# Performance work log

Measured on AMD Instinct MI355X. Metric: run time of the kernel, lower is better.

## Reference

```python
import jax, jax.numpy as jnp
import numpy as np
from jax import lax

N, T, E, A, D, S, O = 64, 2048, 512, 256, 512, 64, 80
R_ATT, R_FAC = 10, 2
H4 = 4 * D  # LSTM hidden size = 2048


def softsign(x):
    return x / (1.0 + jnp.abs(x))


def lstm_cell(x, h, c, Wih, Whh, bih, bhh):
    gates = x @ Wih.T + bih + h @ Whh.T + bhh
    i, f, g, o = jnp.split(gates, 4, axis=-1)  # torch gate order i,f,g,o
    c_new = jax.nn.sigmoid(f) * c + jax.nn.sigmoid(i) * jnp.tanh(g)
    h_new = jax.nn.sigmoid(o) * jnp.tanh(c_new)
    return h_new, c_new


def setup_inputs() -> dict:
    key = jax.random.key(0)
    ks = jax.random.split(key, 24)
    f = lambda k, shape, s=0.05: jax.random.normal(k, shape, dtype=jnp.float32) * s
    return {
        'input_enc': f(ks[0], (N, T, E), 1.0),
        'input_dec': f(ks[1], (N, O), 1.0),
        'spkr_vec': f(ks[2], (N, 1, S), 1.0),
        'speed': jax.random.uniform(ks[3], (N,), dtype=jnp.float32),
        'lengths_enc': jnp.full((N,), T, dtype=jnp.int32),
        'We': f(ks[4], (E, A)), 'be': jnp.zeros((A,), jnp.float32),
        'Ws': f(ks[5], (S, A)),
        'conv_w': f(ks[6], (A, 1, 31)),
        'w_proj': f(ks[7], (A,)), 'b_proj': jnp.zeros((), jnp.float32),
        'W_speed': f(ks[8], (A,)),
        'sp_W1': f(ks[9], (D,)), 'sp_b1': jnp.zeros((D,), jnp.float32),
        'sp_W2': f(ks[10], (D, E)), 'sp_b2': jnp.zeros((E,), jnp.float32),
        'pre_W1': f(ks[11], (O + S, 2 * D)), 'pre_b1': jnp.zeros((2 * D,), jnp.float32),
        'pre_W2': f(ks[12], (2 * D, D)), 'pre_b2': jnp.zeros((D,), jnp.float32),
        'Wih0': f(ks[13], (4 * H4, E + D + S)), 'Whh0': f(ks[14], (4 * H4, H4)),
        'bih0': jnp.zeros((4 * H4,), jnp.float32), 'bhh0': jnp.zeros((4 * H4,), jnp.float32),
        'Wih1': f(ks[15], (4 * H4, H4)), 'Whh1': f(ks[16], (4 * H4, H4)),
        'bih1': jnp.zeros((4 * H4,), jnp.float32), 'bhh1': jnp.zeros((4 * H4,), jnp.float32),
        'Wo': f(ks[17], (H4 + E, O * R_FAC)), 'bo': jnp.zeros((O * R_FAC,), jnp.float32),
    }


def _forward(input_enc, input_dec, spkr_vec, speed, lengths_enc,
             We, be, Ws, conv_w, w_proj, b_proj, W_speed,
             sp_W1, sp_b1, sp_W2, sp_b2,
             pre_W1, pre_b1, pre_W2, pre_b2,
             Wih0, Whh0, bih0, bhh0, Wih1, Whh1, bih1, bhh1, Wo, bo):
    n, t_enc, _ = input_enc.shape
    # first decoding step: previous attention = one-hot at t=0
    att0 = jnp.zeros((n, t_enc), jnp.float32).at[:, 0].set(1.0)
    bias_speed = (speed[:, None] * W_speed[None, :])[:, None, :]            # (N,1,A)
    bias_enc = softsign(jnp.einsum('nte,ea->nta', input_enc, We) + be)      # (N,T,A)
    bias_spkr = softsign(jnp.einsum('nse,ea->nsa', spkr_vec, Ws))           # (N,1,A)
    # prenet (dropout = identity at inference)
    x = jnp.concatenate([input_dec, spkr_vec[:, 0, :]], axis=-1)
    p = jax.nn.relu(jax.nn.relu(x @ pre_W1 + pre_b1) @ pre_W2 + pre_b2)     # (N,D)
    out_prenet = p[:, None, :]
    # location feature: conv1d(1->A, k=31, pad=15) over previous attention
    conv = lax.conv_general_dilated(att0[:, None, :], conv_w, (1,), [(15, 15)],
                                    dimension_numbers=('NCH', 'OIH', 'NCH'))
    conv = conv.transpose(0, 2, 1)                                          # (N,T,A)
    e = bias_enc + bias_spkr + conv + bias_speed                            # (N,T,A)
    # sliding-window mask around previous argmax, indices clamped to [0, len-1]
    m = jnp.argmax(att0, axis=1)                                            # (N,)
    L1 = (lengths_enc - 1).astype(m.dtype)
    i = jnp.arange(R_ATT)
    up = jnp.minimum(m[:, None] + i, L1[:, None])
    lo = jnp.minimum(jnp.maximum(m[:, None] - i, 0), L1[:, None])
    idx = jnp.concatenate([up, lo], axis=1)                                 # (N,2R)
    mask = jnp.zeros((n, t_enc), jnp.float32).at[jnp.arange(n)[:, None], idx].set(1.0)
    logit = jnp.einsum('nta,a->nt', jnp.tanh(e), w_proj) + b_proj           # (N,T)
    w = jnp.exp(logit - jnp.max(logit, axis=1, keepdims=True)) * mask
    att = w / jnp.maximum(jnp.sum(w, axis=1, keepdims=True), 1e-12)         # L1 normalize
    # speed-conditioned encoder shift
    sp = jnp.tanh(jax.nn.relu(speed[:, None] * sp_W1 + sp_b1) @ sp_W2 + sp_b2)  # (N,E)
    enc = input_enc + sp[:, None, :]
    context = jnp.einsum('nt,nte->ne', att, enc)[:, None, :]                # (N,1,E)
    in_lstm = jnp.concatenate([out_prenet, context, spkr_vec], axis=2)[:, 0, :]
    h0 = jnp.zeros((n, H4), jnp.float32)
    h1, _ = lstm_cell(in_lstm, h0, h0, Wih0, Whh0, bih0, bhh0)
    h2, _ = lstm_cell(h1, h0, h0, Wih1, Whh1, bih1, bhh1)
    dec_output = jnp.concatenate([h2[:, None, :], context], axis=2)         # (N,1,H4+E)
    output = (dec_output @ Wo + bo).reshape(n, R_FAC, -1)                   # (N,r,O)
    return output, context, dec_output


def reference(input_enc, input_dec, spkr_vec, speed, lengths_enc,
              We, be, Ws, conv_w, w_proj, b_proj, W_speed,
              sp_W1, sp_b1, sp_W2, sp_b2,
              pre_W1, pre_b1, pre_W2, pre_b2,
              Wih0, Whh0, bih0, bhh0, Wih1, Whh1, bih1, bhh1, Wo, bo):
    return _forward(input_enc, input_dec, spkr_vec, speed, lengths_enc,
                    We, be, Ws, conv_w, w_proj, b_proj, W_speed,
                    sp_W1, sp_b1, sp_W2, sp_b2,
                    pre_W1, pre_b1, pre_W2, pre_b2,
                    Wih0, Whh0, bih0, bhh0, Wih1, Whh1, bih1, bhh1, Wo, bo)
```

## Files before the change

kernel.cpp:

```cpp
#include <hip/hip_runtime.h>
#include <math.h>


__device__ __forceinline__ float sigmoidf_(float x){ return 1.0f/(1.0f+expf(-x)); }
__device__ __forceinline__ float softsignf_(float x){ return x/(1.0f+fabsf(x)); }

__device__ __forceinline__ void llds16(const float* g, float* l)
{
    __builtin_amdgcn_global_load_lds(
        (const __attribute__((address_space(1))) unsigned int*)g,
        (__attribute__((address_space(3))) unsigned int*)l, 16, 0, 0);
}


__global__ void hidden_kernel(const float* __restrict__ input_dec, const float* __restrict__ spkr,
                              const float* __restrict__ W, const float* __restrict__ b,
                              float* __restrict__ hid)
{
    const int n = blockIdx.x;
    const int j = blockIdx.y * 256 + threadIdx.x;
    float a0=0.f, a1=0.f, a2=0.f, a3=0.f;
    #pragma unroll 4
    for (int k = 0; k < 144; k += 4) {
        const float x0 = (k+0 < 80) ? input_dec[n*80 + k+0] : spkr[n*64 + (k+0-80)];
        const float x1 = (k+1 < 80) ? input_dec[n*80 + k+1] : spkr[n*64 + (k+1-80)];
        const float x2 = (k+2 < 80) ? input_dec[n*80 + k+2] : spkr[n*64 + (k+2-80)];
        const float x3 = (k+3 < 80) ? input_dec[n*80 + k+3] : spkr[n*64 + (k+3-80)];
        a0 = fmaf(x0, W[(k+0)*1024 + j], a0);
        a1 = fmaf(x1, W[(k+1)*1024 + j], a1);
        a2 = fmaf(x2, W[(k+2)*1024 + j], a2);
        a3 = fmaf(x3, W[(k+3)*1024 + j], a3);
    }
    hid[n*1024 + j] = fmaxf((a0+a1)+(a2+a3) + b[j], 0.f);
}

__global__ void sp_kernel(const float* __restrict__ speed, const float* __restrict__ sp_W1,
                          const float* __restrict__ sp_b1, const float* __restrict__ sp_W2,
                          const float* __restrict__ sp_b2, float* __restrict__ sp)
{
    const int n = blockIdx.x;
    const int j = blockIdx.y * 256 + threadIdx.x;
    const float s = speed[n];
    float a0=0.f, a1=0.f, a2=0.f, a3=0.f;
    #pragma unroll 4
    for (int d = 0; d < 512; d += 4) {
        const float r0 = fmaxf(fmaf(s, sp_W1[d+0], sp_b1[d+0]), 0.f);
        const float r1 = fmaxf(fmaf(s, sp_W1[d+1], sp_b1[d+1]), 0.f);
        const float r2 = fmaxf(fmaf(s, sp_W1[d+2], sp_b1[d+2]), 0.f);
        const float r3 = fmaxf(fmaf(s, sp_W1[d+3], sp_b1[d+3]), 0.f);
        a0 = fmaf(r0, sp_W2[(d+0)*512 + j], a0);
        a1 = fmaf(r1, sp_W2[(d+1)*512 + j], a1);
        a2 = fmaf(r2, sp_W2[(d+2)*512 + j], a2);
        a3 = fmaf(r3, sp_W2[(d+3)*512 + j], a3);
    }
    sp[n*512 + j] = tanhf((a0+a1)+(a2+a3) + sp_b2[j]);
}

__global__ void p_kernel(const float* __restrict__ hid, const float* __restrict__ W,
                         const float* __restrict__ b, float* __restrict__ xT0)
{
    const int n = blockIdx.x;
    const int j = blockIdx.y * 256 + threadIdx.x;
    const float* xr = hid + n*1024;
    float a0=0.f, a1=0.f, a2=0.f, a3=0.f;
    #pragma unroll 4
    for (int k = 0; k < 1024; k += 4) {
        a0 = fmaf(xr[k+0], W[(k+0)*512 + j], a0);
        a1 = fmaf(xr[k+1], W[(k+1)*512 + j], a1);
        a2 = fmaf(xr[k+2], W[(k+2)*512 + j], a2);
        a3 = fmaf(xr[k+3], W[(k+3)*512 + j], a3);
    }
    xT0[j*64 + n] = fmaxf((a0+a1)+(a2+a3) + b[j], 0.f);
}

__global__ void attn_kernel(const float* __restrict__ input_enc,
                            const float* __restrict__ spkr,
                            const float* __restrict__ speed,
                            const int*   __restrict__ lengths,
                            const float* __restrict__ We,
                            const float* __restrict__ be,
                            const float* __restrict__ Ws,
                            const float* __restrict__ conv_w,
                            const float* __restrict__ w_proj,
                            const float* __restrict__ b_proj,
                            const float* __restrict__ W_speed,
                            const float* __restrict__ sp,
                            float* __restrict__ xT0,
                            float* __restrict__ out_ctx,
                            float* __restrict__ out_dec)
{
    const int n = blockIdx.x;
    const int a = threadIdx.x;
    __shared__ float encs[10*512];
    __shared__ float part[4][10];
    __shared__ float logit_s[10];
    __shared__ float att_s[10];

    const int L1 = lengths[n] - 1;
    const int tc = (L1 + 1 < 10) ? (L1 + 1) : 10;
    const float sn = speed[n];
    const float* enc_n = input_enc + (size_t)n * (2048*512);

    for (int idx = a; idx < 10*512; idx += 256) encs[idx] = enc_n[idx];
    __syncthreads();

    float ds = 0.f;
    for (int s = 0; s < 64; ++s) ds = fmaf(spkr[n*64 + s], Ws[s*256 + a], ds);
    const float bspkr = softsignf_(ds);
    const float bspd  = sn * W_speed[a];
    const float bea   = be[a];
    const float wpa   = w_proj[a];

    float dt[10];
    #pragma unroll
    for (int t = 0; t < 10; ++t) dt[t] = 0.f;
    for (int k = 0; k < 512; ++k) {
        const float w = We[k*256 + a];
        #pragma unroll
        for (int t = 0; t < 10; ++t) dt[t] = fmaf(encs[t*512 + k], w, dt[t]);
    }

    for (int t = 0; t < 10; ++t) {
        float e = softsignf_(dt[t] + bea);
        e += bspkr + conv_w[a*31 + (15 - t)] + bspd;
        float v = tanhf(e) * wpa;
        #pragma unroll
        for (int off = 32; off > 0; off >>= 1) v += __shfl_down(v, off);
        if ((a & 63) == 0) part[a >> 6][t] = v;
    }
    __syncthreads();
    if (a < 10) logit_s[a] = part[0][a] + part[1][a] + part[2][a] + part[3][a] + b_proj[0];
    __syncthreads();
    if (a == 0) {
        float mx = -1e30f;
        for (int t = 0; t < tc; ++t) mx = fmaxf(mx, logit_s[t]);
        float ssum = 0.f;
        for (int t = 0; t < tc; ++t) { att_s[t] = expf(logit_s[t] - mx); ssum += att_s[t]; }
        const float inv = 1.f / fmaxf(ssum, 1e-12f);
        for (int t = 0; t < tc; ++t) att_s[t] *= inv;
        for (int t = tc; t < 10; ++t) att_s[t] = 0.f;
    }
    __syncthreads();

    for (int e0 = a; e0 < 512; e0 += 256) {
        const float spv = sp[n*512 + e0];
        float c = 0.f;
        for (int t = 0; t < tc; ++t) c = fmaf(att_s[t], encs[t*512 + e0] + spv, c);
        xT0[(512 + e0)*64 + n] = c;
        out_ctx[n*512 + e0]   = c;
        out_dec[n*2560 + 2048 + e0] = c;
    }
    if (a < 64) xT0[(1024 + a)*64 + n] = spkr[n*64 + a];
}

#define FMA_ROW(acc, wv) do { \
    acc.x = fmaf(wv.x, xk0.x, acc.x); acc.y = fmaf(wv.x, xk0.y, acc.y); \
    acc.z = fmaf(wv.x, xk0.z, acc.z); acc.w = fmaf(wv.x, xk0.w, acc.w); \
    acc.x = fmaf(wv.y, xk1.x, acc.x); acc.y = fmaf(wv.y, xk1.y, acc.y); \
    acc.z = fmaf(wv.y, xk1.z, acc.z); acc.w = fmaf(wv.y, xk1.w, acc.w); \
    acc.x = fmaf(wv.z, xk2.x, acc.x); acc.y = fmaf(wv.z, xk2.y, acc.y); \
    acc.z = fmaf(wv.z, xk2.z, acc.z); acc.w = fmaf(wv.z, xk2.w, acc.w); \
    acc.x = fmaf(wv.w, xk3.x, acc.x); acc.y = fmaf(wv.w, xk3.y, acc.y); \
    acc.z = fmaf(wv.w, xk3.z, acc.z); acc.w = fmaf(wv.w, xk3.w, acc.w); \
} while(0)

template<int K>
__global__ __launch_bounds__(256, 2)
void gemm_tile(const float* __restrict__ xT, const float* __restrict__ W,
               float* __restrict__ part)
{
    __shared__ __align__(16) float Wl[2][64*64];
    __shared__ __align__(16) float Xl[2][64*64];
    const int tid  = threadIdx.x;
    const int lane = tid & 63;
    const int w    = tid >> 6;
    const int tx   = tid & 15;
    const int ty   = tid >> 4;
    const int jjbase = blockIdx.x * 64;
    const int sy     = blockIdx.y;
    const int jg     = jjbase + ((jjbase >= 2048) ? 2048 : 0);

    constexpr int NT = K / 64;
    constexpr int NTQ = NT / 4, NTR = NT % 4;
    const int tn = NTQ + (sy < NTR ? 1 : 0);
    const int t0 = sy * NTQ + (sy < NTR ? sy : NTR);

    float4 a0 = {0,0,0,0}, a1 = {0,0,0,0}, a2 = {0,0,0,0}, a3 = {0,0,0,0};

    auto stage = [&](int t, int b) {
        const int k0 = t * 64;
        #pragma unroll
        for (int c = 0; c < 4; ++c) {
            const int u = w * 4 + c;
            llds16(xT + (size_t)k0 * 64 + u * 256 + lane * 4, &Xl[b][u * 256]);
            const int r0 = u * 4;
            llds16(W + (size_t)(jg + r0 + (lane >> 4)) * K + k0 + (lane & 15) * 4,
                   &Wl[b][r0 * 64]);
        }
    };

    stage(t0, 0);
    __syncthreads();

    for (int tt = 0; tt < tn; ++tt) {
        const int cur = tt & 1;
        if (tt + 1 < tn) stage(t0 + tt + 1, cur ^ 1);
        const float* Wc = Wl[cur];
        const float* Xc = Xl[cur];
        #pragma unroll
        for (int kk = 0; kk < 64; kk += 4) {
            const float4 xk0 = *(const float4*)(Xc + (kk+0)*64 + tx*4);
            const float4 xk1 = *(const float4*)(Xc + (kk+1)*64 + tx*4);
            const float4 xk2 = *(const float4*)(Xc + (kk+2)*64 + tx*4);
            const float4 xk3 = *(const float4*)(Xc + (kk+3)*64 + tx*4);
            const float4 w0 = *(const float4*)(Wc + (ty*4+0)*64 + kk);
            FMA_ROW(a0, w0);
            const float4 w1 = *(const float4*)(Wc + (ty*4+1)*64 + kk);
            FMA_ROW(a1, w1);
            const float4 w2 = *(const float4*)(Wc + (ty*4+2)*64 + kk);
            FMA_ROW(a2, w2);
            const float4 w3 = *(const float4*)(Wc + (ty*4+3)*64 + kk);
            FMA_ROW(a3, w3);
        }
        __syncthreads();
    }

    float* op = part + (size_t)(sy * 6144 + jjbase) * 64;
    *(float4*)(op + (ty*4+0)*64 + tx*4) = a0;
    *(float4*)(op + (ty*4+1)*64 + tx*4) = a1;
    *(float4*)(op + (ty*4+2)*64 + tx*4) = a2;
    *(float4*)(op + (ty*4+3)*64 + tx*4) = a3;
}

__global__ void lstm_act_kernel(const float* __restrict__ part,
                                const float* __restrict__ b1, const float* __restrict__ b2,
                                float* __restrict__ hT, float* __restrict__ dec_out)
{
    const int idx = blockIdx.x * 256 + threadIdx.x;
    const int n = idx & 63;
    const int m = idx >> 6;
    float gi = b1[m]        + b2[m];
    float gg = b1[4096 + m] + b2[4096 + m];
    float go = b1[6144 + m] + b2[6144 + m];
    #pragma unroll
    for (int s = 0; s < 4; ++s) {
        gi += part[(size_t)(s * 6144 +        m) * 64 + n];
        gg += part[(size_t)(s * 6144 + 2048 + m) * 64 + n];
        go += part[(size_t)(s * 6144 + 4096 + m) * 64 + n];
    }
    const float c = sigmoidf_(gi) * tanhf(gg);
    const float h = sigmoidf_(go) * tanhf(c);
    hT[idx] = h;
    if (dec_out) dec_out[n*2560 + m] = h;
}

__global__ void final_partial_kernel(const float* __restrict__ h2T, const float* __restrict__ ctx,
                                     const float* __restrict__ Wo, float* __restrict__ part)
{
    const int n  = blockIdx.x;
    const int kc = blockIdx.y;
    const int j  = threadIdx.x;
    if (j >= 160) return;
    const int k0 = kc * 128;
    float a0=0.f, a1=0.f, a2=0.f, a3=0.f;
    if (kc < 16) {
        #pragma unroll 4
        for (int k = k0; k < k0 + 128; k += 4) {
            a0 = fmaf(h2T[(k+0)*64 + n], Wo[(k+0)*160 + j], a0);
            a1 = fmaf(h2T[(k+1)*64 + n], Wo[(k+1)*160 + j], a1);
            a2 = fmaf(h2T[(k+2)*64 + n], Wo[(k+2)*160 + j], a2);
            a3 = fmaf(h2T[(k+3)*64 + n], Wo[(k+3)*160 + j], a3);
        }
    } else {
        const float* cr = ctx + n*512;
        #pragma unroll 4
        for (int k = k0; k < k0 + 128; k += 4) {
            a0 = fmaf(cr[k+0-2048], Wo[(k+0)*160 + j], a0);
            a1 = fmaf(cr[k+1-2048], Wo[(k+1)*160 + j], a1);
            a2 = fmaf(cr[k+2-2048], Wo[(k+2)*160 + j], a2);
            a3 = fmaf(cr[k+3-2048], Wo[(k+3)*160 + j], a3);
        }
    }
    part[(kc*64 + n)*160 + j] = (a0+a1)+(a2+a3);
}

__global__ void final_reduce_kernel(const float* __restrict__ part, const float* __restrict__ bo,
                                    float* __restrict__ out)
{
    const int idx = blockIdx.x * 256 + threadIdx.x;
    const int j = idx - (idx / 160) * 160;
    float s = bo[j];
    #pragma unroll
    for (int kc = 0; kc < 20; ++kc) s += part[kc*10240 + idx];
    out[idx] = s;
}

extern "C" void kernel_launch(void* const* d_in, const int* in_sizes, int n_in,
                              void* d_out, int out_size, void* d_ws, size_t ws_size,
                              hipStream_t stream)
{
    const float* input_enc = (const float*)d_in[0];
    const float* input_dec = (const float*)d_in[1];
    const float* spkr      = (const float*)d_in[2];
    const float* speed     = (const float*)d_in[3];
    const int*   lengths   = (const int*)  d_in[4];
    const float* We        = (const float*)d_in[5];
    const float* be        = (const float*)d_in[6];
    const float* Ws        = (const float*)d_in[7];
    const float* conv_w    = (const float*)d_in[8];
    const float* w_proj    = (const float*)d_in[9];
    const float* b_proj    = (const float*)d_in[10];
    const float* W_speed   = (const float*)d_in[11];
    const float* sp_W1     = (const float*)d_in[12];
    const float* sp_b1     = (const float*)d_in[13];
    const float* sp_W2     = (const float*)d_in[14];
    const float* sp_b2     = (const float*)d_in[15];
    const float* pre_W1    = (const float*)d_in[16];
    const float* pre_b1    = (const float*)d_in[17];
    const float* pre_W2    = (const float*)d_in[18];
    const float* pre_b2    = (const float*)d_in[19];
    const float* Wih0      = (const float*)d_in[20];
    const float* bih0      = (const float*)d_in[22];
    const float* bhh0      = (const float*)d_in[23];
    const float* Wih1      = (const float*)d_in[24];
    const float* bih1      = (const float*)d_in[26];
    const float* bhh1      = (const float*)d_in[27];
    const float* Wo        = (const float*)d_in[28];
    const float* bo        = (const float*)d_in[29];

    float* ws  = (float*)d_ws;
    float* XT0  = ws;
    float* PART = ws + 69632;
    float* XT1  = ws + 1642496;
    float* HID  = ws + 1773568;
    float* SP   = ws + 1839104;
    float* FPART= ws + 69632;

    float* out     = (float*)d_out;
    float* out_ctx = out + 10240;
    float* out_dec = out + 43008;

    hidden_kernel<<<dim3(64,4), 256, 0, stream>>>(input_dec, spkr, pre_W1, pre_b1, HID);
    sp_kernel<<<dim3(64,2), 256, 0, stream>>>(speed, sp_W1, sp_b1, sp_W2, sp_b2, SP);
    p_kernel<<<dim3(64,2), 256, 0, stream>>>(HID, pre_W2, pre_b2, XT0);
    attn_kernel<<<64, 256, 0, stream>>>(input_enc, spkr, speed, lengths, We, be, Ws, conv_w,
                                        w_proj, b_proj, W_speed, SP, XT0, out_ctx, out_dec);
    gemm_tile<1088><<<dim3(96,4), 256, 0, stream>>>(XT0, Wih0, PART);
    lstm_act_kernel<<<512, 256, 0, stream>>>(PART, bih0, bhh0, XT1, nullptr);
    gemm_tile<2048><<<dim3(96,4), 256, 0, stream>>>(XT1, Wih1, PART);
    lstm_act_kernel<<<512, 256, 0, stream>>>(PART, bih1, bhh1, XT1, out_dec);
    final_partial_kernel<<<dim3(64,20), 256, 0, stream>>>(XT1, out_ctx, Wo, FPART);
    final_reduce_kernel<<<40, 256, 0, stream>>>(FPART, bo, out);
}
```

Measured before the change: 668.6 us.

## Rewrite LSTM gate GEMM to hold activations in registers with 8-way K split

Result: no change. 667.8 us (-0.1%).

```diff
diff --git a/kernel.cpp b/kernel.cpp
--- a/kernel.cpp
+++ b/kernel.cpp
@@ -153,83 +153,83 @@
     if (a < 64) xT0[(1024 + a)*64 + n] = spkr[n*64 + a];
 }
 
-#define FMA_ROW(acc, wv) do { \
-    acc.x = fmaf(wv.x, xk0.x, acc.x); acc.y = fmaf(wv.x, xk0.y, acc.y); \
-    acc.z = fmaf(wv.x, xk0.z, acc.z); acc.w = fmaf(wv.x, xk0.w, acc.w); \
-    acc.x = fmaf(wv.y, xk1.x, acc.x); acc.y = fmaf(wv.y, xk1.y, acc.y); \
-    acc.z = fmaf(wv.y, xk1.z, acc.z); acc.w = fmaf(wv.y, xk1.w, acc.w); \
-    acc.x = fmaf(wv.z, xk2.x, acc.x); acc.y = fmaf(wv.z, xk2.y, acc.y); \
-    acc.z = fmaf(wv.z, xk2.z, acc.z); acc.w = fmaf(wv.z, xk2.w, acc.w); \
-    acc.x = fmaf(wv.w, xk3.x, acc.x); acc.y = fmaf(wv.w, xk3.y, acc.y); \
-    acc.z = fmaf(wv.w, xk3.z, acc.z); acc.w = fmaf(wv.w, xk3.w, acc.w); \
-} while(0)
-
-template<int K>
-__global__ __launch_bounds__(256, 2)
-void gemm_tile(const float* __restrict__ xT, const float* __restrict__ W,
-               float* __restrict__ part)
-{
-    __shared__ __align__(16) float Wl[2][64*64];
-    __shared__ __align__(16) float Xl[2][64*64];
+template<int K, int S>
+__global__ __launch_bounds__(256, 3)
+void gemm_bx(const float* __restrict__ xT, const float* __restrict__ W,
+             float* __restrict__ part)
+{
+    __shared__ __align__(16) float Wl0[64*64];
+    __shared__ __align__(16) float Wl1[64*64];
     const int tid  = threadIdx.x;
     const int lane = tid & 63;
-    const int w    = tid >> 6;
-    const int tx   = tid & 15;
-    const int ty   = tid >> 4;
+    const int wv   = tid >> 6;
     const int jjbase = blockIdx.x * 64;
     const int sy     = blockIdx.y;
     const int jg     = jjbase + ((jjbase >= 2048) ? 2048 : 0);
 
-    constexpr int NT = K / 64;
-    constexpr int NTQ = NT / 4, NTR = NT % 4;
+    constexpr int NT  = K / 64;
+    constexpr int NTQ = NT / S, NTR = NT % S;
     const int tn = NTQ + (sy < NTR ? 1 : 0);
     const int t0 = sy * NTQ + (sy < NTR ? sy : NTR);
 
-    float4 a0 = {0,0,0,0}, a1 = {0,0,0,0}, a2 = {0,0,0,0}, a3 = {0,0,0,0};
-
-    auto stage = [&](int t, int b) {
+    float acc[16];
+    #pragma unroll
+    for (int i = 0; i < 16; ++i) acc[i] = 0.f;
+
+    auto stage = [&](int t, float* Wl) {
         const int k0 = t * 64;
         #pragma unroll
         for (int c = 0; c < 4; ++c) {
-            const int u = w * 4 + c;
-            llds16(xT + (size_t)k0 * 64 + u * 256 + lane * 4, &Xl[b][u * 256]);
-            const int r0 = u * 4;
+            const int r0 = (wv * 4 + c) * 4;
             llds16(W + (size_t)(jg + r0 + (lane >> 4)) * K + k0 + (lane & 15) * 4,
-                   &Wl[b][r0 * 64]);
+                   Wl + r0 * 64);
         }
     };
 
-    stage(t0, 0);
-    __syncthreads();
-
+    float xv[64];
+
+    stage(t0, Wl0);
+    {
+        const int k0 = t0 * 64;
+        #pragma unroll
+        for (int i = 0; i < 64; ++i) xv[i] = xT[(size_t)(k0 + i) * 64 + lane];
+    }
+    __syncthreads();
+
+    const float* Wc = Wl0;
+    float* Wn = Wl1;
     for (int tt = 0; tt < tn; ++tt) {
-        const int cur = tt & 1;
-        if (tt + 1 < tn) stage(t0 + tt + 1, cur ^ 1);
-        const float* Wc = Wl[cur];
-        const float* Xc = Xl[cur];
-        #pragma unroll
-        for (int kk = 0; kk < 64; kk += 4) {
-            const float4 xk0 = *(const float4*)(Xc + (kk+0)*64 + tx*4);
-            const float4 xk1 = *(const float4*)(Xc + (kk+1)*64 + tx*4);
-            const float4 xk2 = *(const float4*)(Xc + (kk+2)*64 + tx*4);
-            const float4 xk3 = *(const float4*)(Xc + (kk+3)*64 + tx*4);
-            const float4 w0 = *(const float4*)(Wc + (ty*4+0)*64 + kk);
-            FMA_ROW(a0, w0);
-            const float4 w1 = *(const float4*)(Wc + (ty*4+1)*64 + kk);
-            FMA_ROW(a1, w1);
-            const float4 w2 = *(const float4*)(Wc + (ty*4+2)*64 + kk);
-            FMA_ROW(a2, w2);
-            const float4 w3 = *(const float4*)(Wc + (ty*4+3)*64 + kk);
-            FMA_ROW(a3, w3);
+        if (tt > 0) {
+            const int k0 = (t0 + tt) * 64;
+            #pragma unroll
+            for (int i = 0; i < 64; ++i) xv[i] = xT[(size_t)(k0 + i) * 64 + lane];
+        }
+        if (tt + 1 < tn) stage(t0 + tt + 1, Wn);
+
+        #pragma unroll
+        for (int jp = 0; jp < 16; jp += 2) {
+            const float* W0 = Wc + (wv * 16 + jp) * 64;
+            const float* W1 = W0 + 64;
+            float aA = 0.f, aB = 0.f;
+            #pragma unroll
+            for (int kk = 0; kk < 64; kk += 4) {
+                const float4 wa = *(const float4*)(W0 + kk);
+                const float4 wb = *(const float4*)(W1 + kk);
+                aA = fmaf(wa.x, xv[kk+0], aA);  aB = fmaf(wb.x, xv[kk+0], aB);
+                aA = fmaf(wa.y, xv[kk+1], aA);  aB = fmaf(wb.y, xv[kk+1], aB);
+                aA = fmaf(wa.z, xv[kk+2], aA);  aB = fmaf(wb.z, xv[kk+2], aB);
+                aA = fmaf(wa.w, xv[kk+3], aA);  aB = fmaf(wb.w, xv[kk+3], aB);
+            }
+            acc[jp]   += aA;
+            acc[jp+1] += aB;
         }
         __syncthreads();
-    }
-
-    float* op = part + (size_t)(sy * 6144 + jjbase) * 64;
-    *(float4*)(op + (ty*4+0)*64 + tx*4) = a0;
-    *(float4*)(op + (ty*4+1)*64 + tx*4) = a1;
-    *(float4*)(op + (ty*4+2)*64 + tx*4) = a2;
-    *(float4*)(op + (ty*4+3)*64 + tx*4) = a3;
+        float* t_ = (float*)Wc; Wc = Wn; Wn = t_;
+    }
+
+    float* op = part + (size_t)(sy * 6144 + jjbase + wv * 16) * 64 + lane;
+    #pragma unroll
+    for (int jj = 0; jj < 16; ++jj) op[jj * 64] = acc[jj];
 }
 
 __global__ void lstm_act_kernel(const float* __restrict__ part,
@@ -243,7 +243,7 @@
     float gg = b1[4096 + m] + b2[4096 + m];
     float go = b1[6144 + m] + b2[6144 + m];
     #pragma unroll
-    for (int s = 0; s < 4; ++s) {
+    for (int s = 0; s < 8; ++s) {
         gi += part[(size_t)(s * 6144 +        m) * 64 + n];
         gg += part[(size_t)(s * 6144 + 2048 + m) * 64 + n];
         go += part[(size_t)(s * 6144 + 4096 + m) * 64 + n];
@@ -328,12 +328,12 @@
     const float* Wo        = (const float*)d_in[28];
     const float* bo        = (const float*)d_in[29];
 
-    float* ws  = (float*)d_ws;
+    float* ws   = (float*)d_ws;
     float* XT0  = ws;
     float* PART = ws + 69632;
-    float* XT1  = ws + 1642496;
-    float* HID  = ws + 1773568;
-    float* SP   = ws + 1839104;
+    float* XT1  = ws + 3215360;
+    float* HID  = ws + 3346432;
+    float* SP   = ws + 3411968;
     float* FPART= ws + 69632;
 
     float* out     = (float*)d_out;
@@ -345,9 +345,9 @@
     p_kernel<<<dim3(64,2), 256, 0, stream>>>(HID, pre_W2, pre_b2, XT0);
     attn_kernel<<<64, 256, 0, stream>>>(input_enc, spkr, speed, lengths, We, be, Ws, conv_w,
                                         w_proj, b_proj, W_speed, SP, XT0, out_ctx, out_dec);
-    gemm_tile<1088><<<dim3(96,4), 256, 0, stream>>>(XT0, Wih0, PART);
+    gemm_bx<1088, 8><<<dim3(96,8), 256, 0, stream>>>(XT0, Wih0, PART);
     lstm_act_kernel<<<512, 256, 0, stream>>>(PART, bih0, bhh0, XT1, nullptr);
-    gemm_tile<2048><<<dim3(96,4), 256, 0, stream>>>(XT1, Wih1, PART);
+    gemm_bx<2048, 8><<<dim3(96,8), 256, 0, stream>>>(XT1, Wih1, PART);
     lstm_act_kernel<<<512, 256, 0, stream>>>(PART, bih1, bhh1, XT1, out_dec);
     final_partial_kernel<<<dim3(64,20), 256, 0, stream>>>(XT1, out_ctx, Wo, FPART);
     final_reduce_kernel<<<40, 256, 0, stream>>>(FPART, bo, out);
```
